# Optimization experiments

Measured on AMD Instinct MI355X. Metric: run time of the kernel, lower is better.

Reference implementation:

```python
import jax, jax.numpy as jnp
import numpy as np


def setup_inputs() -> dict:
    key = jax.random.key(0)
    ks = jax.random.split(key, 10)
    B, S, D = 16, 2048, 256
    return {
        "x": jax.random.normal(ks[0], (B, S, D), dtype=jnp.float32),
        "noise": jax.random.normal(ks[1], (B, S, D), dtype=jnp.float32),
        "alpha1": jax.random.normal(ks[2], (D,), dtype=jnp.float32),
        "alpha2": jax.random.normal(ks[3], (D,), dtype=jnp.float32),
        "W_ttt": jax.random.normal(ks[4], (D, D), dtype=jnp.float32),
        "W_proj": jax.random.normal(ks[5], (D, D), dtype=jnp.float32),
        "ff_alpha": jax.random.normal(ks[6], (D,), dtype=jnp.float32),
        "ff_beta": jax.random.normal(ks[7], (D,), dtype=jnp.float32),
        "ff_gamma": jax.random.normal(ks[8], (1,), dtype=jnp.float32),
        "ff_eta": jax.random.normal(ks[9], (1,), dtype=jnp.float32),
    }


def _ttt(W, m, noise):
    # m, noise: [B, S, D]; sequential SGD on W over the sequence axis.
    B, S, D = m.shape
    scale = 2.0 / (B * D)  # d(mse)/d(pred) factor

    def step(W, inp):
        state, eps = inp                      # [B, D] each
        train = state + eps
        diff = train @ W.T - state            # pred - label, [B, D]
        grad = scale * (diff.T @ train)       # dL/dW, [D, D]
        Wn = W - 0.01 * grad
        return Wn, state @ Wn.T               # readout with updated W

    _, outs = jax.lax.scan(step, W, (jnp.swapaxes(m, 0, 1), jnp.swapaxes(noise, 0, 1)))
    return jnp.swapaxes(outs, 0, 1)           # [B, S, D]


def reference(x, noise, alpha1, alpha2, W_ttt, W_proj, ff_alpha, ff_beta, ff_gamma, ff_eta):
    # memory path: VecDyT norm then TTT (readouts are detached in torch)
    m = jnp.tanh(alpha1 * x)
    mem = jax.lax.stop_gradient(_ttt(W_ttt, m, noise))

    # feedforward path: VecDyT norm then FFUnit
    v = jnp.tanh(alpha2 * x)
    u = ff_gamma * jax.nn.gelu(ff_alpha * v, approximate=False) + ff_eta * jnp.sin(ff_beta * v)
    g = u * (v @ W_proj.T)

    return mem + g
```

## Files before the change

kernel.cpp:

```cpp
#include <hip/hip_runtime.h>

typedef unsigned short u16;
typedef unsigned int u32;
typedef __attribute__((ext_vector_type(8))) short bf16x8;
typedef __attribute__((ext_vector_type(4))) float f32x4;

#define SB 16
#define SS 2048
#define SD 256
#define CC 16
#define NCH (SS / CC)
#define KAPPA 4.8828125e-6f
#define RP 24
#define SLOT 65536

__device__ __forceinline__ u16 f2bf(float f) {
  u32 u = __float_as_uint(f);
  u = (u + 0x7FFFu + ((u >> 16) & 1u)) >> 16;
  return (u16)u;
}
__device__ __forceinline__ float bf2f(u16 u) { return __uint_as_float((u32)u << 16); }

__device__ __forceinline__ bf16x8 ldfrag(const u16* p) {
  union { uint4 u; bf16x8 f; } cv;
  cv.u = *(const uint4*)p;
  return cv.f;
}
__device__ __forceinline__ bf16x8 asfrag(uint4 q) {
  union { uint4 u; bf16x8 f; } cv;
  cv.u = q;
  return cv.f;
}
__device__ __forceinline__ f32x4 mfma16(bf16x8 a, bf16x8 b, f32x4 c) {
  return __builtin_amdgcn_mfma_f32_16x16x32_bf16(a, b, c, 0, 0, 0);
}

__global__ __launch_bounds__(256) void prep_kernel(
    const float* __restrict__ x, const float* __restrict__ noise,
    const float* __restrict__ a1, const float* __restrict__ a2,
    u16* __restrict__ train, u16* __restrict__ state, u16* __restrict__ trainT,
    u16* __restrict__ vh, u16* __restrict__ vl) {
  size_t i4 = (size_t)blockIdx.x * 256 + threadIdx.x;
  size_t base = i4 * 4;
  int d = (int)(base & 255);
  int t = (int)((base >> 8) & 2047);
  int b = (int)(base >> 19);
  float4 xv = *(const float4*)(x + base);
  float4 nv = *(const float4*)(noise + base);
  float4 av = *(const float4*)(a1 + d);
  float4 a2v = *(const float4*)(a2 + d);
  float m0 = tanhf(av.x * xv.x);
  float m1 = tanhf(av.y * xv.y);
  float m2 = tanhf(av.z * xv.z);
  float m3 = tanhf(av.w * xv.w);
  size_t dst = ((size_t)t * SB + b) * SD + d;
  ushort4 tr, st;
  tr.x = f2bf(m0 + nv.x); tr.y = f2bf(m1 + nv.y);
  tr.z = f2bf(m2 + nv.z); tr.w = f2bf(m3 + nv.w);
  st.x = f2bf(m0); st.y = f2bf(m1); st.z = f2bf(m2); st.w = f2bf(m3);
  *(ushort4*)(train + dst) = tr;
  *(ushort4*)(state + dst) = st;
  size_t tb = ((size_t)t * SD + d) * SB + b;
  trainT[tb + 0 * SB] = tr.x;
  trainT[tb + 1 * SB] = tr.y;
  trainT[tb + 2 * SB] = tr.z;
  trainT[tb + 3 * SB] = tr.w;
  float v0 = tanhf(a2v.x * xv.x);
  float v1 = tanhf(a2v.y * xv.y);
  float v2 = tanhf(a2v.z * xv.z);
  float v3 = tanhf(a2v.w * xv.w);
  ushort4 h, l;
  h.x = f2bf(v0); l.x = f2bf(v0 - bf2f(h.x));
  h.y = f2bf(v1); l.y = f2bf(v1 - bf2f(h.y));
  h.z = f2bf(v2); l.z = f2bf(v2 - bf2f(h.z));
  h.w = f2bf(v3); l.w = f2bf(v3 - bf2f(h.w));
  *(ushort4*)(vh + base) = h;
  *(ushort4*)(vl + base) = l;
}

__global__ __launch_bounds__(256) void wsplit_kernel(
    const float* __restrict__ Wp, u16* __restrict__ Wph, u16* __restrict__ Wpl) {
  size_t i = ((size_t)blockIdx.x * 256 + threadIdx.x) * 4;
  float4 v = *(const float4*)(Wp + i);
  ushort4 h, l;
  h.x = f2bf(v.x); l.x = f2bf(v.x - bf2f(h.x));
  h.y = f2bf(v.y); l.y = f2bf(v.y - bf2f(h.y));
  h.z = f2bf(v.z); l.z = f2bf(v.z - bf2f(h.z));
  h.w = f2bf(v.w); l.w = f2bf(v.w - bf2f(h.w));
  *(ushort4*)(Wph + i) = h;
  *(ushort4*)(Wpl + i) = l;
}

__global__ __launch_bounds__(256) void gram2ff_kernel(
    const u16* __restrict__ tr, const u16* __restrict__ st,
    u16* __restrict__ AG, u16* __restrict__ LbG,
    const u16* __restrict__ vh, const u16* __restrict__ vl,
    const u16* __restrict__ Wph, const u16* __restrict__ Wpl,
    const float* __restrict__ ffa, const float* __restrict__ ffb,
    const float* __restrict__ ffg_, const float* __restrict__ ffe_,
    float* __restrict__ out) {
  const int tid = threadIdx.x;

  if (blockIdx.x < 2048) {
    const int id = blockIdx.x;
    const int c = (id & 7) + 8 * (id >> 7);
    const int t = (id >> 3) & 15;
    const int cb = c * 16 + t;
    const int lane = tid & 63, wv = tid >> 6;
    const int lr = lane & 15, lq = lane >> 4;
    const size_t Tt = (size_t)cb;
    bf16x8 trF[8], stF[8];
#pragma unroll
    for (int k = 0; k < 8; ++k) {
      trF[k] = ldfrag(tr + (Tt * 16 + lr) * 256 + k * 32 + lq * 8);
      stF[k] = ldfrag(st + (Tt * 16 + lr) * 256 + k * 32 + lq * 8);
    }
    for (int ii = 0; ii < 2; ++ii) {
      const int sp = wv + ii * 4;
      u16* dA = AG + ((size_t)cb * 8 + sp) * 512;
      u16* dL = LbG + ((size_t)cb * 8 + sp) * 512;
#pragma unroll
      for (int h = 0; h < 2; ++h) {
        const int s = 2 * sp + h;
        f32x4 accA = {0.f, 0.f, 0.f, 0.f}, accL = {0.f, 0.f, 0.f, 0.f};
        if (s <= t) {
          const u16* bsrc = tr + ((size_t)(c * 16 + s) * 16 + lr) * 256 + lq * 8;
#pragma unroll
          for (int k = 0; k < 8; ++k) {
            bf16x8 bk = ldfrag(bsrc + k * 32);
            if (s < t) accA = mfma16(trF[k], bk, accA);
            accL = mfma16(stF[k], bk, accL);
          }
        }
#pragma unroll
        for (int r = 0; r < 4; ++r) {
          int idx = (lq * 4 + r) * 32 + h * 16 + lr;
          dA[idx] = (s < t) ? f2bf(accA[r]) : (u16)0;
          dL[idx] = (s <= t) ? f2bf(accL[r]) : (u16)0;
        }
      }
    }
    return;
  }

  const int fb = blockIdx.x - 2048;
  const int gm0 = ((fb & 7) + 8 * (fb >> 5)) * 64;
  const int gn0 = ((fb >> 3) & 3) * 64;
  const int lane = tid & 63, w = tid >> 6;
  const int lr = lane & 15, lq = lane >> 4;

  bf16x8 ah[8], al[8];
  {
    const u16* vhp = vh + (size_t)(gm0 + w * 16 + lr) * 256 + lq * 8;
    const u16* vlp = vl + (size_t)(gm0 + w * 16 + lr) * 256 + lq * 8;
#pragma unroll
    for (int kb = 0; kb < 8; ++kb) {
      ah[kb] = ldfrag(vhp + kb * 32);
      al[kb] = ldfrag(vlp + kb * 32);
    }
  }
  const float ga = ffg_[0], et = ffe_[0];
#pragma unroll
  for (int cb = 0; cb < 4; ++cb) {
    const u16* bhp = Wph + (size_t)(gn0 + cb * 16 + lr) * 256 + lq * 8;
    const u16* blp = Wpl + (size_t)(gn0 + cb * 16 + lr) * 256 + lq * 8;
    f32x4 acc = {0.f, 0.f, 0.f, 0.f};
#pragma unroll
    for (int kb = 0; kb < 8; ++kb) {
      bf16x8 bh = ldfrag(bhp + kb * 32);
      bf16x8 bl = ldfrag(blp + kb * 32);
      acc = mfma16(ah[kb], bh, acc);
      acc = mfma16(al[kb], bh, acc);
      acc = mfma16(ah[kb], bl, acc);
    }
#pragma unroll
    for (int r = 0; r < 4; ++r) {
      const int row = gm0 + w * 16 + lq * 4 + r;
      const int col = gn0 + cb * 16 + lr;
      const size_t vi = (size_t)row * 256 + col;
      float v = bf2f(vh[vi]) + bf2f(vl[vi]);
      float z = ffa[col] * v;
      float gelu = 0.5f * z * (1.0f + erff(z * 0.70710678118654752f));
      float u = ga * gelu + et * sinf(ffb[col] * v);
      out[vi] = u * acc[r];
    }
  }
}

__global__ __launch_bounds__(512) void phaseA_kernel(
    const u16* __restrict__ tr, const u16* __restrict__ st,
    const u16* __restrict__ trT, const u16* __restrict__ AG,
    u16* __restrict__ Dt, u16* __restrict__ Db, u16* __restrict__ Qb) {
  __shared__ u16 StT[CC][16 * RP];
  __shared__ u16 YtL[CC][16 * RP];
  __shared__ u16 ZtL[CC][16 * RP];
  const int tid = threadIdx.x;
  const int lane = tid & 63;
  const int w = tid >> 6;
  const int id = blockIdx.x;
  const int c = (id & 7) + 8 * (id >> 7);
  const int d1b = (id >> 3) & 15;
  const int lr = lane & 15;
  const int lq = lane >> 4;

  uint4 agR[2][8];
#pragma unroll
  for (int u = 0; u < 2; ++u) {
    const u16* ag = AG + ((size_t)(c * 16 + w + 8 * u) * 8) * 512 + lr * 32 + lq * 8;
#pragma unroll
    for (int sp = 0; sp < 8; ++sp) agR[u][sp] = *(const uint4*)(ag + sp * 512);
  }
  u16 sraw[2][4];
  float xs[2][4];
#pragma unroll
  for (int u = 0; u < 2; ++u) {
    const size_t T = (size_t)c * CC + w + 8 * u;
    ushort4 pk;
#pragma unroll
    for (int r = 0; r < 4; ++r) {
      size_t idx = (T * 16 + lq * 4 + r) * 256 + d1b * 16 + lr;
      sraw[u][r] = st[idx];
      xs[u][r] = bf2f(tr[idx]);
      ((u16*)&pk)[r] = sraw[u][r];
    }
    *(ushort4*)(&StT[w + 8 * u][lr * RP + lq * 4]) = pk;
  }
  __syncthreads();

#pragma unroll
  for (int u = 0; u < 2; ++u) {
    f32x4 a1 = {0.f, 0.f, 0.f, 0.f}, a2 = {0.f, 0.f, 0.f, 0.f};
#pragma unroll
    for (int sp = 0; sp < 8; ++sp) {
      const int s0 = 2 * sp + (lq >> 1);
      bf16x8 xb = ldfrag(trT + ((size_t)(c * CC + s0) * 256 + d1b * 16 + lr) * 16 +
                         (lq & 1) * 8);
      bf16x8 sb = ldfrag(&StT[s0][lr * RP + (lq & 1) * 8]);
      a1 = mfma16(asfrag(agR[u][sp]), xb, a1);
      a2 = mfma16(asfrag(agR[u][sp]), sb, a2);
    }
    ushort4 py, pz;
#pragma unroll
    for (int r = 0; r < 4; ++r) {
      ((u16*)&py)[r] = f2bf(xs[u][r] - KAPPA * a1[r]);
      ((u16*)&pz)[r] = f2bf(bf2f(sraw[u][r]) - KAPPA * a2[r]);
    }
    *(ushort4*)(&YtL[w + 8 * u][lr * RP + lq * 4]) = py;
    *(ushort4*)(&ZtL[w + 8 * u][lr * RP + lq * 4]) = pz;
  }
  __syncthreads();

  bf16x8 yf[8], zf[8];
#pragma unroll
  for (int sp = 0; sp < 8; ++sp) {
    yf[sp] = ldfrag(&YtL[2 * sp + (lq >> 1)][lr * RP + (lq & 1) * 8]);
    zf[sp] = ldfrag(&ZtL[2 * sp + (lq >> 1)][lr * RP + (lq & 1) * 8]);
  }
  const size_t base = (size_t)c * SLOT;
#pragma unroll
  for (int u = 0; u < 2; ++u) {
    const int d2b = w + 8 * u;
    f32x4 da = {0.f, 0.f, 0.f, 0.f}, qa = {0.f, 0.f, 0.f, 0.f};
#pragma unroll
    for (int sp = 0; sp < 8; ++sp) {
      bf16x8 xb = ldfrag(trT + ((size_t)(c * CC + 2 * sp + (lq >> 1)) * 256 +
                                d2b * 16 + lr) * 16 + (lq & 1) * 8);
      da = mfma16(yf[sp], xb, da);
      qa = mfma16(zf[sp], xb, qa);
    }
    ushort4 dpk;
#pragma unroll
    for (int r = 0; r < 4; ++r) {
      const u16 dv = f2bf(-KAPPA * da[r]);
      ((u16*)&dpk)[r] = dv;
      Db[base + (size_t)(d1b * 16 + lq * 4 + r) * 256 + d2b * 16 + lr] = dv;
      Qb[base + (size_t)(d1b * 16 + lq * 4 + r) * 256 + d2b * 16 + lr] =
          f2bf(KAPPA * qa[r]);
    }
    *(ushort4*)(Dt + base + (size_t)(d2b * 16 + lr) * 256 + d1b * 16 + lq * 4) = dpk;
  }
}

__global__ __launch_bounds__(512) void klev_kernel(
    u16* __restrict__ Dt, u16* __restrict__ Db, u16* __restrict__ Qb, int lev) {
  __shared__ u16 S[65536];
  const int qn = blockIdx.x;
  const int half = 1 << (lev - 1);
  const int blk = qn >> (lev - 1), win = qn & (half - 1);
  const int i = blk * half * 2 + half + win;
  const int j = blk * half * 2 + half - 1;
  u16* Dti = Dt + (size_t)i * SLOT;
  const u16* Dtj = Dt + (size_t)j * SLOT;
  u16* Dbi = Db + (size_t)i * SLOT;
  const u16* Dbj = Db + (size_t)j * SLOT;
  u16* Qi = Qb + (size_t)i * SLOT;
  const u16* Qj = Qb + (size_t)j * SLOT;
  const int tid = threadIdx.x;
  const int lane = tid & 63, w = tid >> 6;
  const int lr = lane & 15, lq = lane >> 4;

  for (int it = tid; it < 8192; it += 512) {
    int row = it >> 5, c16 = it & 31;
    uint4 v = *(const uint4*)(Dti + (size_t)row * 256 + c16 * 8);
    int off = row * 512 + ((c16 * 16) ^ ((row & 7) << 4));
    *(uint4*)((char*)S + off) = v;
  }
  __syncthreads();

#pragma unroll
  for (int ui = 0; ui < 2; ++ui) {
    const int rb = w + 8 * ui;
    bf16x8 aq[8];
#pragma unroll
    for (int kb = 0; kb < 8; ++kb)
      aq[kb] = ldfrag(Qj + (size_t)(rb * 16 + lr) * 256 + kb * 32 + lq * 8);
    for (int cb = 0; cb < 16; ++cb) {
      f32x4 acc = {0.f, 0.f, 0.f, 0.f};
#pragma unroll
      for (int kb = 0; kb < 8; ++kb) {
        const int row = cb * 16 + lr;
        const int colb = kb * 64 + lq * 16;
        bf16x8 bf = *(const bf16x8*)((const char*)S + row * 512 +
                                     (colb ^ ((row & 7) << 4)));
        acc = mfma16(aq[kb], bf, acc);
      }
#pragma unroll
      for (int r = 0; r < 4; ++r) {
        size_t idx = (size_t)(rb * 16 + lq * 4 + r) * 256 + cb * 16 + lr;
        Qi[idx] = f2bf(acc[r] + bf2f(Qj[idx]) + bf2f(Qi[idx]));
      }
    }
  }
  bf16x8 ad[2][8];
#pragma unroll
  for (int ui = 0; ui < 2; ++ui) {
    const int rb = w + 8 * ui;
#pragma unroll
    for (int kb = 0; kb < 8; ++kb) {
      const int row = rb * 16 + lr;
      const int colb = kb * 64 + lq * 16;
      ad[ui][kb] = *(const bf16x8*)((const char*)S + row * 512 +
                                    (colb ^ ((row & 7) << 4)));
    }
  }
  __syncthreads();

  for (int it = tid; it < 8192; it += 512) {
    int row = it >> 5, c16 = it & 31;
    uint4 v = *(const uint4*)(Dbj + (size_t)row * 256 + c16 * 8);
    int off = row * 512 + ((c16 * 16) ^ ((row & 7) << 4));
    *(uint4*)((char*)S + off) = v;
  }
  __syncthreads();

#pragma unroll
  for (int ui = 0; ui < 2; ++ui) {
    const int rb = w + 8 * ui;
    for (int cb = 0; cb < 16; ++cb) {
      f32x4 acc = {0.f, 0.f, 0.f, 0.f};
#pragma unroll
      for (int kb = 0; kb < 8; ++kb) {
        const int row = cb * 16 + lr;
        const int colb = kb * 64 + lq * 16;
        bf16x8 bf = *(const bf16x8*)((const char*)S + row * 512 +
                                     (colb ^ ((row & 7) << 4)));
        acc = mfma16(ad[ui][kb], bf, acc);
      }
      ushort4 mir;
#pragma unroll
      for (int r = 0; r < 4; ++r) {
        size_t idx = (size_t)(rb * 16 + lq * 4 + r) * 256 + cb * 16 + lr;
        const u16 nv = f2bf(acc[r] + bf2f(Dtj[idx]) + bf2f(Dti[idx]));
        ((u16*)&mir)[r] = nv;
        Dti[idx] = nv;
      }
      *(ushort4*)(Dbi + (size_t)(cb * 16 + lr) * 256 + rb * 16 + lq * 4) = mir;
    }
  }
}

__global__ __launch_bounds__(512) void wstart_kernel(
    const float* __restrict__ Wttt, const u16* __restrict__ Dt,
    const u16* __restrict__ Qb, u16* __restrict__ Wsb) {
  const int c = blockIdx.x;
  const int tid = threadIdx.x;
  const int lane = tid & 63, w = tid >> 6;
  const int lr = lane & 15, lq = lane >> 4;
  if (c == 0) {
    for (int i = tid; i < SLOT / 4; i += 512) {
      float4 v = *(const float4*)(Wttt + (size_t)i * 4);
      ushort4 o;
      o.x = f2bf(v.x); o.y = f2bf(v.y); o.z = f2bf(v.z); o.w = f2bf(v.w);
      *(ushort4*)(Wsb + (size_t)i * 4) = o;
    }
    return;
  }
  const size_t ex = (size_t)(c - 1) * SLOT;
  u16* Wc = Wsb + (size_t)c * SLOT;
#pragma unroll
  for (int ui = 0; ui < 2; ++ui) {
    const int rb = w + 8 * ui;
    bf16x8 wf[8];
#pragma unroll
    for (int kb = 0; kb < 8; ++kb) {
      const float* wp = Wttt + (size_t)(rb * 16 + lr) * 256 + kb * 32 + lq * 8;
      float4 w0 = *(const float4*)(wp);
      float4 w1 = *(const float4*)(wp + 4);
      union { u16 s[8]; bf16x8 f; } cv;
      cv.s[0] = f2bf(w0.x); cv.s[1] = f2bf(w0.y);
      cv.s[2] = f2bf(w0.z); cv.s[3] = f2bf(w0.w);
      cv.s[4] = f2bf(w1.x); cv.s[5] = f2bf(w1.y);
      cv.s[6] = f2bf(w1.z); cv.s[7] = f2bf(w1.w);
      wf[kb] = cv.f;
    }
    for (int cb = 0; cb < 16; ++cb) {
      f32x4 acc = {0.f, 0.f, 0.f, 0.f};
#pragma unroll
      for (int kb = 0; kb < 8; ++kb) {
        bf16x8 bf = ldfrag(Dt + ex + (size_t)(cb * 16 + lr) * 256 + kb * 32 + lq * 8);
        acc = mfma16(wf[kb], bf, acc);
      }
#pragma unroll
      for (int r = 0; r < 4; ++r) {
        size_t idx = (size_t)(rb * 16 + lq * 4 + r) * 256 + cb * 16 + lr;
        float v = Wttt[idx] + acc[r] + bf2f(Qb[ex + idx]);
        Wc[idx] = f2bf(v);
      }
    }
  }
}

__global__ __launch_bounds__(512) void phaseC_kernel(
    const u16* __restrict__ tr, const u16* __restrict__ st,
    const u16* __restrict__ AG, const u16* __restrict__ LbG,
    const u16* __restrict__ Wsb, float* __restrict__ out) {
  __shared__ u16 RpL[CC][16 * RP];
  __shared__ u16 DpL[CC][16 * RP];
  __shared__ u16 WbL[16][268];

  const int tid = threadIdx.x;
  const int lane = tid & 63;
  const int w = tid >> 6;
  const int id = blockIdx.x;
  const int c = (id & 7) + 8 * (id >> 7);
  const int d1b = (id >> 3) & 15;
  const int lr = lane & 15;
  const int lq = lane >> 4;

  {
    const int row = tid >> 5, col = (tid & 31) * 8;
    *(uint4*)&WbL[row][col] =
        *(const uint4*)(Wsb + (size_t)c * SLOT + (size_t)(d1b * 16 + row) * 256 + col);
  }
  __syncthreads();

  uint4 agR[2][8];
#pragma unroll
  for (int u = 0; u < 2; ++u) {
    const u16* ag = AG + ((size_t)(c * 16 + w + 8 * u) * 8) * 512 + lr * 32 + lq * 8;
#pragma unroll
    for (int sp = 0; sp < 8; ++sp) agR[u][sp] = *(const uint4*)(ag + sp * 512);
  }
  uint4 trR[2][8], stR[2][8];
  float sub[2][4];
#pragma unroll
  for (int u = 0; u < 2; ++u) {
    const size_t T = (size_t)c * CC + w + 8 * u;
    const u16* trt = tr + (T * 16 + lr) * 256 + lq * 8;
    const u16* stt = st + (T * 16 + lr) * 256 + lq * 8;
#pragma unroll
    for (int k = 0; k < 8; ++k) {
      trR[u][k] = *(const uint4*)(trt + k * 32);
      stR[u][k] = *(const uint4*)(stt + k * 32);
    }
#pragma unroll
    for (int r = 0; r < 4; ++r)
      sub[u][r] = bf2f(st[(T * 16 + lq * 4 + r) * 256 + d1b * 16 + lr]);
  }

  f32x4 rhsF[2], qF[2];
#pragma unroll
  for (int u = 0; u < 2; ++u) {
    f32x4 racc = {0.f, 0.f, 0.f, 0.f}, qacc = {0.f, 0.f, 0.f, 0.f};
#pragma unroll
    for (int k = 0; k < 8; ++k) {
      bf16x8 wb = ldfrag(&WbL[lr][k * 32 + lq * 8]);
      racc = mfma16(asfrag(trR[u][k]), wb, racc);
      qacc = mfma16(asfrag(stR[u][k]), wb, qacc);
    }
#pragma unroll
    for (int r = 0; r < 4; ++r) racc[r] -= sub[u][r];
    rhsF[u] = racc; qF[u] = qacc;
    ushort4 pk;
    pk.x = f2bf(racc.x); pk.y = f2bf(racc.y);
    pk.z = f2bf(racc.z); pk.w = f2bf(racc.w);
    *(ushort4*)(&RpL[w + 8 * u][lr * RP + lq * 4]) = pk;
  }
  __syncthreads();

  uint4 lbR[2][8];
#pragma unroll
  for (int u = 0; u < 2; ++u) {
    const u16* lb = LbG + ((size_t)(c * 16 + w + 8 * u) * 8) * 512 + lr * 32 + lq * 8;
#pragma unroll
    for (int sp = 0; sp < 8; ++sp) lbR[u][sp] = *(const uint4*)(lb + sp * 512);
  }

#pragma unroll
  for (int u = 0; u < 2; ++u) {
    f32x4 acc = {0.f, 0.f, 0.f, 0.f};
#pragma unroll
    for (int sp = 0; sp < 8; ++sp) {
      bf16x8 bf = ldfrag(&RpL[2 * sp + (lq >> 1)][lr * RP + (lq & 1) * 8]);
      acc = mfma16(asfrag(agR[u][sp]), bf, acc);
    }
    ushort4 pk;
#pragma unroll
    for (int r = 0; r < 4; ++r) {
      float dv = rhsF[u][r] - KAPPA * acc[r];
      ((u16*)&pk)[r] = f2bf(-KAPPA * dv);
    }
    *(ushort4*)(&DpL[w + 8 * u][lr * RP + lq * 4]) = pk;
  }
  __syncthreads();

  float gp[2][4];
#pragma unroll
  for (int u = 0; u < 2; ++u) {
    const size_t T = (size_t)c * CC + w + 8 * u;
#pragma unroll
    for (int r = 0; r < 4; ++r)
      gp[u][r] = out[((size_t)(lq * 4 + r) * SS + T) * SD + d1b * 16 + lr];
  }
#pragma unroll
  for (int u = 0; u < 2; ++u) {
    const size_t T = (size_t)c * CC + w + 8 * u;
    f32x4 acc = qF[u];
#pragma unroll
    for (int sp = 0; sp < 8; ++sp) {
      bf16x8 bf = ldfrag(&DpL[2 * sp + (lq >> 1)][lr * RP + (lq & 1) * 8]);
      acc = mfma16(asfrag(lbR[u][sp]), bf, acc);
    }
#pragma unroll
    for (int r = 0; r < 4; ++r) {
      size_t oi = ((size_t)(lq * 4 + r) * SS + T) * SD + d1b * 16 + lr;
      out[oi] = acc[r] + gp[u][r];
    }
  }
}

extern "C" void kernel_launch(void* const* d_in, const int* in_sizes, int n_in,
                              void* d_out, int out_size, void* d_ws, size_t ws_size,
                              hipStream_t stream) {
  const float* x     = (const float*)d_in[0];
  const float* noise = (const float*)d_in[1];
  const float* a1    = (const float*)d_in[2];
  const float* a2    = (const float*)d_in[3];
  const float* Wttt  = (const float*)d_in[4];
  const float* Wproj = (const float*)d_in[5];
  const float* ffa   = (const float*)d_in[6];
  const float* ffb   = (const float*)d_in[7];
  const float* ffg   = (const float*)d_in[8];
  const float* ffe   = (const float*)d_in[9];
  float* out = (float*)d_out;

  const size_t N = (size_t)SB * SS * SD;
  u16* tr  = (u16*)d_ws;
  u16* st  = tr + N;
  u16* trT = st + N;
  u16* AG  = trT + N;
  u16* LbG = AG + N;
  u16* Dt  = LbG + N;
  u16* Qb  = Dt + N;
  u16* Db  = Qb + N;
  u16* Wsb = trT;
  u16* vhB = Dt;
  u16* vlB = Qb;
  u16* Wph = Db;
  u16* Wpl = Db + SLOT;

  prep_kernel<<<8192, 256, 0, stream>>>(x, noise, a1, a2, tr, st, trT, vhB, vlB);
  wsplit_kernel<<<64, 256, 0, stream>>>(Wproj, Wph, Wpl);
  gram2ff_kernel<<<4096, 256, 0, stream>>>(tr, st, AG, LbG, vhB, vlB, Wph, Wpl,
                                           ffa, ffb, ffg, ffe, out);
  phaseA_kernel<<<2048, 512, 0, stream>>>(tr, st, trT, AG, Dt, Db, Qb);
  for (int lev = 1; lev <= 7; ++lev)
    klev_kernel<<<64, 512, 0, stream>>>(Dt, Db, Qb, lev);
  wstart_kernel<<<128, 512, 0, stream>>>(Wttt, Dt, Qb, Wsb);
  phaseC_kernel<<<2048, 512, 0, stream>>>(tr, st, AG, LbG, Wsb, out);
}
```

Measured before the change: 1.004 ms.

## Merge the level kernels into one cooperative kernel split across more blocks

```diff
diff --git a/kernel.cpp b/kernel.cpp
--- a/kernel.cpp
+++ b/kernel.cpp
@@ -1,4 +1,7 @@
 #include <hip/hip_runtime.h>
+#include <hip/hip_cooperative_groups.h>
+
+namespace cg = cooperative_groups;
 
 typedef unsigned short u16;
 typedef unsigned int u32;
@@ -281,40 +284,46 @@
   }
 }
 
-__global__ __launch_bounds__(512) void klev_kernel(
-    u16* __restrict__ Dt, u16* __restrict__ Db, u16* __restrict__ Qb, int lev) {
+__global__ __launch_bounds__(512) void klev_coop(
+    u16* __restrict__ Dt, u16* __restrict__ Db, u16* __restrict__ Qb) {
   __shared__ u16 S[65536];
-  const int qn = blockIdx.x;
-  const int half = 1 << (lev - 1);
-  const int blk = qn >> (lev - 1), win = qn & (half - 1);
-  const int i = blk * half * 2 + half + win;
-  const int j = blk * half * 2 + half - 1;
-  u16* Dti = Dt + (size_t)i * SLOT;
-  const u16* Dtj = Dt + (size_t)j * SLOT;
-  u16* Dbi = Db + (size_t)i * SLOT;
-  const u16* Dbj = Db + (size_t)j * SLOT;
-  u16* Qi = Qb + (size_t)i * SLOT;
-  const u16* Qj = Qb + (size_t)j * SLOT;
+  cg::grid_group grid = cg::this_grid();
   const int tid = threadIdx.x;
   const int lane = tid & 63, w = tid >> 6;
   const int lr = lane & 15, lq = lane >> 4;
-
-  for (int it = tid; it < 8192; it += 512) {
-    int row = it >> 5, c16 = it & 31;
-    uint4 v = *(const uint4*)(Dti + (size_t)row * 256 + c16 * 8);
-    int off = row * 512 + ((c16 * 16) ^ ((row & 7) << 4));
-    *(uint4*)((char*)S + off) = v;
-  }
-  __syncthreads();
-
-#pragma unroll
-  for (int ui = 0; ui < 2; ++ui) {
-    const int rb = w + 8 * ui;
+  const int qn = blockIdx.x & 63;
+  const int rbg = blockIdx.x >> 6;
+  const int rb = rbg * 4 + (w & 3);
+  const int ch = w >> 2;
+
+  for (int lev = 1; lev <= 7; ++lev) {
+    const int half = 1 << (lev - 1);
+    const int blk = qn >> (lev - 1), win = qn & (half - 1);
+    const int i = blk * half * 2 + half + win;
+    const int j = blk * half * 2 + half - 1;
+    u16* Dti = Dt + (size_t)i * SLOT;
+    const u16* Dtj = Dt + (size_t)j * SLOT;
+    u16* Dbi = Db + (size_t)i * SLOT;
+    const u16* Dbj = Db + (size_t)j * SLOT;
+    u16* Qi = Qb + (size_t)i * SLOT;
+    const u16* Qj = Qb + (size_t)j * SLOT;
+
+    for (int it = tid; it < 8192; it += 512) {
+      int row = it >> 5, c16 = it & 31;
+      uint4 v = *(const uint4*)(Dti + (size_t)row * 256 + c16 * 8);
+      int off = row * 512 + ((c16 * 16) ^ ((row & 7) << 4));
+      *(uint4*)((char*)S + off) = v;
+    }
+    __syncthreads();
+
     bf16x8 aq[8];
 #pragma unroll
     for (int kb = 0; kb < 8; ++kb)
       aq[kb] = ldfrag(Qj + (size_t)(rb * 16 + lr) * 256 + kb * 32 + lq * 8);
-    for (int cb = 0; cb < 16; ++cb) {
+    float oldv[8][4];
+#pragma unroll
+    for (int cc = 0; cc < 8; ++cc) {
+      const int cb = cc * 2 + ch;
       f32x4 acc = {0.f, 0.f, 0.f, 0.f};
 #pragma unroll
       for (int kb = 0; kb < 8; ++kb) {
@@ -328,35 +337,31 @@
       for (int r = 0; r < 4; ++r) {
         size_t idx = (size_t)(rb * 16 + lq * 4 + r) * 256 + cb * 16 + lr;
         Qi[idx] = f2bf(acc[r] + bf2f(Qj[idx]) + bf2f(Qi[idx]));
+        oldv[cc][r] = bf2f(Dtj[idx]) + bf2f(Dti[idx]);
       }
     }
-  }
-  bf16x8 ad[2][8];
-#pragma unroll
-  for (int ui = 0; ui < 2; ++ui) {
-    const int rb = w + 8 * ui;
+    bf16x8 ad[8];
 #pragma unroll
     for (int kb = 0; kb < 8; ++kb) {
       const int row = rb * 16 + lr;
       const int colb = kb * 64 + lq * 16;
-      ad[ui][kb] = *(const bf16x8*)((const char*)S + row * 512 +
-                                    (colb ^ ((row & 7) << 4)));
-    }
-  }
-  __syncthreads();
-
-  for (int it = tid; it < 8192; it += 512) {
-    int row = it >> 5, c16 = it & 31;
-    uint4 v = *(const uint4*)(Dbj + (size_t)row * 256 + c16 * 8);
-    int off = row * 512 + ((c16 * 16) ^ ((row & 7) << 4));
-    *(uint4*)((char*)S + off) = v;
-  }
-  __syncthreads();
-
-#pragma unroll
-  for (int ui = 0; ui < 2; ++ui) {
-    const int rb = w + 8 * ui;
-    for (int cb = 0; cb < 16; ++cb) {
+      ad[kb] = *(const bf16x8*)((const char*)S + row * 512 +
+                                (colb ^ ((row & 7) << 4)));
+    }
+    __threadfence();
+    grid.sync();
+
+    for (int it = tid; it < 8192; it += 512) {
+      int row = it >> 5, c16 = it & 31;
+      uint4 v = *(const uint4*)(Dbj + (size_t)row * 256 + c16 * 8);
+      int off = row * 512 + ((c16 * 16) ^ ((row & 7) << 4));
+      *(uint4*)((char*)S + off) = v;
+    }
+    __syncthreads();
+
+#pragma unroll
+    for (int cc = 0; cc < 8; ++cc) {
+      const int cb = cc * 2 + ch;
       f32x4 acc = {0.f, 0.f, 0.f, 0.f};
 #pragma unroll
       for (int kb = 0; kb < 8; ++kb) {
@@ -364,18 +369,21 @@
         const int colb = kb * 64 + lq * 16;
         bf16x8 bf = *(const bf16x8*)((const char*)S + row * 512 +
                                      (colb ^ ((row & 7) << 4)));
-        acc = mfma16(ad[ui][kb], bf, acc);
+        acc = mfma16(ad[kb], bf, acc);
       }
       ushort4 mir;
 #pragma unroll
       for (int r = 0; r < 4; ++r) {
         size_t idx = (size_t)(rb * 16 + lq * 4 + r) * 256 + cb * 16 + lr;
-        const u16 nv = f2bf(acc[r] + bf2f(Dtj[idx]) + bf2f(Dti[idx]));
+        const u16 nv = f2bf(acc[r] + oldv[cc][r]);
         ((u16*)&mir)[r] = nv;
         Dti[idx] = nv;
       }
       *(ushort4*)(Dbi + (size_t)(cb * 16 + lr) * 256 + rb * 16 + lq * 4) = mir;
     }
+    __threadfence();
+    grid.sync();
+    __syncthreads();
   }
 }
 
@@ -584,8 +592,11 @@
   gram2ff_kernel<<<4096, 256, 0, stream>>>(tr, st, AG, LbG, vhB, vlB, Wph, Wpl,
                                            ffa, ffb, ffg, ffe, out);
   phaseA_kernel<<<2048, 512, 0, stream>>>(tr, st, trT, AG, Dt, Db, Qb);
-  for (int lev = 1; lev <= 7; ++lev)
-    klev_kernel<<<64, 512, 0, stream>>>(Dt, Db, Qb, lev);
+  {
+    void* args[] = {(void*)&Dt, (void*)&Db, (void*)&Qb};
+    hipLaunchCooperativeKernel((void*)klev_coop, dim3(256), dim3(512), args, 0,
+                               stream);
+  }
   wstart_kernel<<<128, 512, 0, stream>>>(Wttt, Dt, Qb, Wsb);
   phaseC_kernel<<<2048, 512, 0, stream>>>(tr, st, AG, LbG, Wsb, out);
 }
```

After: 1.936 ms. 92.9% more time.
